# Optimization experiments

Measured on AMD Instinct MI355X. Metric: run time of the kernel, lower is better.

The kernel has to match this reference:

```python
import jax, jax.numpy as jnp
import numpy as np

B, T, C, H, O = 64, 256, 2048, 512, 11
THRESHOLD = 1.0
LEAK = 0.003
OUTPUT_LEAK = LEAK * 0.5


def setup_inputs() -> dict:
    key = jax.random.key(0)
    k1, k2, k3, k4 = jax.random.split(key, 4)
    x = jax.random.normal(k1, (B, T, C), dtype=jnp.float32)
    # xavier_uniform(gain=0.1) for fc1: bound = 0.1*sqrt(6/(C+H))
    b1 = 0.1 * np.sqrt(6.0 / (C + H))
    w1 = jax.random.uniform(k2, (H, C), jnp.float32, -b1, b1)
    # orthogonal(gain=0.1) for fc_rec -> approximate with small gaussian scaled like orthogonal rows
    w_rec = 0.1 * jnp.linalg.qr(jax.random.normal(k3, (H, H), jnp.float32))[0]
    b2 = 0.3 * np.sqrt(6.0 / (H + O))
    w2 = jax.random.uniform(k4, (O, H), jnp.float32, -b2, b2)
    return {"x": x, "w1": w1, "w_rec": w_rec, "w2": w2}


def reference(x, w1, w_rec, w2):
    batch, t_steps, _ = x.shape
    n_hidden = w1.shape[0]
    n_output = w2.shape[0]
    dt = x.dtype

    def step(carry, x_t):
        v1, spk1, v2, out_sum = carry
        # input + recurrent current: [B,H]
        i1 = x_t @ w1.T + spk1 @ w_rec.T
        # subtractive LIF: leak, threshold, subtractive reset
        v1 = v1 + i1 - LEAK
        spk = (v1 >= THRESHOLD).astype(dt)
        v1 = v1 - spk * THRESHOLD
        # non-spiking output accumulator neuron: [B,O]
        i2 = spk @ w2.T
        v2 = jnp.maximum(v2 + i2 - OUTPUT_LEAK, 0.0)
        out_sum = out_sum + v2
        return (v1, spk, v2, out_sum), None

    init = (
        jnp.zeros((batch, n_hidden), dt),
        jnp.zeros((batch, n_hidden), dt),
        jnp.zeros((batch, n_output), dt),
        jnp.zeros((batch, n_output), dt),
    )
    (_, _, _, out_sum), _ = jax.lax.scan(step, init, jnp.swapaxes(x, 0, 1))
    return out_sum / t_steps
```

## Files before the change

kernel.cpp:

```cpp
#include <hip/hip_runtime.h>
#include <cstddef>

#define B_ 64
#define T_ 256
#define C_ 2048
#define H_ 512
#define O_ 11
#define THRESH 1.0f
#define LEAK_ 0.003f
#define OLEAK_ 0.0015f

typedef float v2f __attribute__((ext_vector_type(2)));
typedef float v4f __attribute__((ext_vector_type(4)));

__global__ __launch_bounds__(256) void transpose_wrec(const float* __restrict__ w,
                                                      float* __restrict__ wt) {
    __shared__ float tile[32][33];
    int tx = threadIdx.x, ty = threadIdx.y;
    int x = blockIdx.x * 32 + tx;
    int y = blockIdx.y * 32 + ty;
#pragma unroll
    for (int i = 0; i < 32; i += 8)
        tile[ty + i][tx] = w[(size_t)(y + i) * H_ + x];
    __syncthreads();
    int x2 = blockIdx.y * 32 + tx;
    int y2 = blockIdx.x * 32 + ty;
#pragma unroll
    for (int i = 0; i < 32; i += 8)
        wt[(size_t)(y2 + i) * H_ + x2] = tile[tx][ty + i];
}

#define BM 128
#define BN 128
#define BK 16
#define LDT (BM + 4)

template <int S>
__global__ __launch_bounds__(256) void gemm_ff(const float* __restrict__ A,
                                               const float* __restrict__ Bw,
                                               float* __restrict__ Pout) {
    const int K = C_;
    const int N = H_;
    const int kLen = C_ / S;

    const int i  = blockIdx.x + 4 * blockIdx.y + 512 * blockIdx.z;
    const int l  = (i & 7) * (64 * S) + (i >> 3);
    const int bx = l & 3;
    const int by = (l >> 2) & 127;
    const int bz = l >> 9;

    const int kBase = bz * kLen;

    __shared__ float As[BK][LDT];
    __shared__ float Bs[BK][LDT];

    const int t  = threadIdx.x;
    const int tx = t & 15;
    const int ty = t >> 4;
    const int lr = t >> 2;
    const int lc = (t & 3) * 4;

    const float* Ap = A  + (size_t)(by * BM + lr) * K + kBase + lc;
    const float* Bp = Bw + (size_t)(bx * BN + lr) * K + kBase + lc;

    v2f acc[8][4];
#pragma unroll
    for (int ii = 0; ii < 8; ++ii)
#pragma unroll
        for (int j = 0; j < 4; ++j) acc[ii][j] = (v2f){0.f, 0.f};

    float4 a0 = *(const float4*)(Ap);
    float4 a1 = *(const float4*)(Ap + (size_t)64 * K);
    float4 b0 = *(const float4*)(Bp);
    float4 b1 = *(const float4*)(Bp + (size_t)64 * K);

    for (int k0 = 0;;) {
        __syncthreads();
        As[lc + 0][lr] = a0.x; As[lc + 1][lr] = a0.y;
        As[lc + 2][lr] = a0.z; As[lc + 3][lr] = a0.w;
        As[lc + 0][lr + 64] = a1.x; As[lc + 1][lr + 64] = a1.y;
        As[lc + 2][lr + 64] = a1.z; As[lc + 3][lr + 64] = a1.w;
        Bs[lc + 0][lr] = b0.x; Bs[lc + 1][lr] = b0.y;
        Bs[lc + 2][lr] = b0.z; Bs[lc + 3][lr] = b0.w;
        Bs[lc + 0][lr + 64] = b1.x; Bs[lc + 1][lr + 64] = b1.y;
        Bs[lc + 2][lr + 64] = b1.z; Bs[lc + 3][lr + 64] = b1.w;
        __syncthreads();

        k0 += BK;
        const bool more = (k0 < kLen);
        if (more) {
            Ap += BK; Bp += BK;
            a0 = *(const float4*)(Ap);
            a1 = *(const float4*)(Ap + (size_t)64 * K);
            b0 = *(const float4*)(Bp);
            b1 = *(const float4*)(Bp + (size_t)64 * K);
        }

#pragma unroll
        for (int k = 0; k < BK; ++k) {
            float4 alo = *(const float4*)&As[k][ty * 4];
            float4 ahi = *(const float4*)&As[k][64 + ty * 4];
            float4 blo = *(const float4*)&Bs[k][tx * 4];
            float4 bhi = *(const float4*)&Bs[k][64 + tx * 4];
            v2f b0v = {blo.x, blo.y}, b1v = {blo.z, blo.w};
            v2f b2v = {bhi.x, bhi.y}, b3v = {bhi.z, bhi.w};
            float av[8] = {alo.x, alo.y, alo.z, alo.w, ahi.x, ahi.y, ahi.z, ahi.w};
#pragma unroll
            for (int ii = 0; ii < 8; ++ii) {
                v2f ai = {av[ii], av[ii]};
                acc[ii][0] += ai * b0v;
                acc[ii][1] += ai * b1v;
                acc[ii][2] += ai * b2v;
                acc[ii][3] += ai * b3v;
            }
        }
        if (!more) break;
    }

    float* P = Pout + (size_t)bz * ((size_t)B_ * T_ * H_);
#pragma unroll
    for (int ii = 0; ii < 8; ++ii) {
        int row = by * BM + (ii < 4 ? ty * 4 + ii : 64 + ty * 4 + (ii - 4));
        float* Cp = P + (size_t)row * N + bx * BN;
        v4f c0 = {acc[ii][0].x, acc[ii][0].y, acc[ii][1].x, acc[ii][1].y};
        v4f c1 = {acc[ii][2].x, acc[ii][2].y, acc[ii][3].x, acc[ii][3].y};
        __builtin_nontemporal_store(c0, (v4f*)(Cp + tx * 4));
        __builtin_nontemporal_store(c1, (v4f*)(Cp + 64 + tx * 4));
    }
}

template <int S>
__global__ __launch_bounds__(512) void snn_rec(const float* __restrict__ I1,
                                               const float* __restrict__ wrT,
                                               const float* __restrict__ w2,
                                               float* __restrict__ out) {
    const int b    = blockIdx.x;
    const int h    = threadIdx.x;
    const int lane = h & 63;
    const int w    = h >> 6;

    __shared__ float w2sT[H_ * 12];
    __shared__ int   lists[2][H_];
    __shared__ int   wcnt[8];
    __shared__ float v2s[O_];
    __shared__ float osum[O_];

#pragma unroll
    for (int o = 0; o < O_; ++o) w2sT[h * 12 + o] = w2[o * H_ + h];
    if (h < O_) { v2s[h] = 0.f; osum[h] = 0.f; }

    float v1 = 0.f;
    int   pc = 0;
    const float*  i1p  = I1 + (size_t)b * T_ * H_ + h;
    const float*  wr_h = wrT + h;
    const size_t  PARTF = (size_t)B_ * T_ * H_;

    float pfA[S], pfB[S];
#pragma unroll
    for (int s = 0; s < S; ++s) pfA[s] = __builtin_nontemporal_load(i1p + s * PARTF);
#pragma unroll
    for (int s = 0; s < S; ++s) pfB[s] = __builtin_nontemporal_load(i1p + s * PARTF + H_);
    __syncthreads();

    for (int t = 0; t < T_; ++t) {
        const int cur = t & 1;

        float acc = -LEAK_;
        if (cur == 0) {
#pragma unroll
            for (int s = 0; s < S; ++s) acc += pfA[s];
            const size_t tn = (size_t)((t + 2 < T_) ? t + 2 : t);
#pragma unroll
            for (int s = 0; s < S; ++s)
                pfA[s] = __builtin_nontemporal_load(i1p + s * PARTF + tn * H_);
        } else {
#pragma unroll
            for (int s = 0; s < S; ++s) acc += pfB[s];
            const size_t tn = (size_t)((t + 2 < T_) ? t + 2 : t);
#pragma unroll
            for (int s = 0; s < S; ++s)
                pfB[s] = __builtin_nontemporal_load(i1p + s * PARTF + tn * H_);
        }

        const int* pl = lists[cur ^ 1];
        int j = 0;
        for (; j + 15 < pc; j += 16) {
            const int4 ia = *(const int4*)(pl + j);
            const int4 ib = *(const int4*)(pl + j + 4);
            const int4 ic = *(const int4*)(pl + j + 8);
            const int4 id = *(const int4*)(pl + j + 12);
            float g0 = wr_h[ia.x * H_], g1 = wr_h[ia.y * H_];
            float g2 = wr_h[ia.z * H_], g3 = wr_h[ia.w * H_];
            float g4 = wr_h[ib.x * H_], g5 = wr_h[ib.y * H_];
            float g6 = wr_h[ib.z * H_], g7 = wr_h[ib.w * H_];
            float g8 = wr_h[ic.x * H_], g9 = wr_h[ic.y * H_];
            float gA = wr_h[ic.z * H_], gB = wr_h[ic.w * H_];
            float gC = wr_h[id.x * H_], gD = wr_h[id.y * H_];
            float gE = wr_h[id.z * H_], gF = wr_h[id.w * H_];
            acc += g0; acc += g1; acc += g2; acc += g3;
            acc += g4; acc += g5; acc += g6; acc += g7;
            acc += g8; acc += g9; acc += gA; acc += gB;
            acc += gC; acc += gD; acc += gE; acc += gF;
        }
        for (; j + 7 < pc; j += 8) {
            const int4 ia = *(const int4*)(pl + j);
            const int4 ib = *(const int4*)(pl + j + 4);
            float g0 = wr_h[ia.x * H_], g1 = wr_h[ia.y * H_];
            float g2 = wr_h[ia.z * H_], g3 = wr_h[ia.w * H_];
            float g4 = wr_h[ib.x * H_], g5 = wr_h[ib.y * H_];
            float g6 = wr_h[ib.z * H_], g7 = wr_h[ib.w * H_];
            acc += g0; acc += g1; acc += g2; acc += g3;
            acc += g4; acc += g5; acc += g6; acc += g7;
        }
        for (; j < pc; ++j) acc += wr_h[pl[j] * H_];

        v1 += acc;
        const bool spike = (v1 >= THRESH);
        if (spike) v1 -= THRESH;

        unsigned long long m = __ballot(spike);
        int lb = __popcll(m & ((1ull << lane) - 1ull));
        if (lane == 0) wcnt[w] = (int)__popcll(m);
        __syncthreads();

        int base = 0, tot = 0;
#pragma unroll
        for (int ww = 0; ww < 8; ++ww) {
            int c = wcnt[ww];
            if (ww < w) base += c;
            tot += c;
        }
        if (spike) lists[cur][base + lb] = h;
        __syncthreads();

        if (h < O_) {
            const int* cl = lists[cur];
            float s2 = 0.f;
            for (int j2 = 0; j2 < tot; ++j2) s2 += w2sT[cl[j2] * 12 + h];
            float v2 = v2s[h] + s2 - OLEAK_;
            v2 = v2 > 0.f ? v2 : 0.f;
            v2s[h] = v2;
            osum[h] += v2;
        }
        pc = tot;
    }
    __syncthreads();
    if (h < O_) out[b * O_ + h] = osum[h] * (1.0f / (float)T_);
}

extern "C" void kernel_launch(void* const* d_in, const int* in_sizes, int n_in,
                              void* d_out, int out_size, void* d_ws, size_t ws_size,
                              hipStream_t stream) {
    const float* x     = (const float*)d_in[0];
    const float* w1    = (const float*)d_in[1];
    const float* w_rec = (const float*)d_in[2];
    const float* w2    = (const float*)d_in[3];
    float* out = (float*)d_out;

    const size_t PART = (size_t)B_ * T_ * H_ * sizeof(float);
    const size_t WRT  = (size_t)H_ * H_ * sizeof(float);

    int S = 1;
    if (ws_size >= 4 * PART + WRT) S = 4;
    else if (ws_size >= 2 * PART + WRT) S = 2;

    float* P   = (float*)d_ws;
    float* wrT = (float*)((char*)d_ws + (size_t)S * PART);

    transpose_wrec<<<dim3(H_ / 32, H_ / 32), dim3(32, 8), 0, stream>>>(w_rec, wrT);

    dim3 ggrid(H_ / BN, (B_ * T_) / BM, S);
    switch (S) {
        case 4:
            gemm_ff<4><<<ggrid, dim3(256), 0, stream>>>(x, w1, P);
            snn_rec<4><<<dim3(B_), dim3(H_), 0, stream>>>(P, wrT, w2, out);
            break;
        case 2:
            gemm_ff<2><<<ggrid, dim3(256), 0, stream>>>(x, w1, P);
            snn_rec<2><<<dim3(B_), dim3(H_), 0, stream>>>(P, wrT, w2, out);
            break;
        default:
            gemm_ff<1><<<ggrid, dim3(256), 0, stream>>>(x, w1, P);
            snn_rec<1><<<dim3(B_), dim3(H_), 0, stream>>>(P, wrT, w2, out);
            break;
    }
}
```

Measured before the change: 782.7 us.

## Double-buffer GEMM LDS tiles, simplify recurrent prefetch, use LDS-only barriers

The feed-forward GEMM now ping-pongs between two shared-memory tiles, so each k-step needs one barrier instead of two. It also switches the partial-sum stores from nontemporal to regular stores. The recurrent kernel prefetches the input current one step ahead with normal loads instead of two steps ahead with nontemporal loads. It also replaces __syncthreads with a barrier that waits only on LDS counters, to shorten the per-timestep serial latency. The shallower prefetch may expose global-load latency inside the serial time loop.

```diff
diff --git a/kernel.cpp b/kernel.cpp
--- a/kernel.cpp
+++ b/kernel.cpp
@@ -11,7 +11,11 @@
 #define OLEAK_ 0.0015f
 
 typedef float v2f __attribute__((ext_vector_type(2)));
-typedef float v4f __attribute__((ext_vector_type(4)));
+
+__device__ __forceinline__ void lds_barrier() {
+    asm volatile("s_waitcnt lgkmcnt(0)" ::: "memory");
+    __builtin_amdgcn_s_barrier();
+}
 
 __global__ __launch_bounds__(256) void transpose_wrec(const float* __restrict__ w,
                                                       float* __restrict__ wt) {
@@ -48,11 +52,10 @@
     const int bx = l & 3;
     const int by = (l >> 2) & 127;
     const int bz = l >> 9;
-
     const int kBase = bz * kLen;
 
-    __shared__ float As[BK][LDT];
-    __shared__ float Bs[BK][LDT];
+    __shared__ float As[2][BK][LDT];
+    __shared__ float Bs[2][BK][LDT];
 
     const int t  = threadIdx.x;
     const int tx = t & 15;
@@ -74,34 +77,24 @@
     float4 b0 = *(const float4*)(Bp);
     float4 b1 = *(const float4*)(Bp + (size_t)64 * K);
 
-    for (int k0 = 0;;) {
-        __syncthreads();
-        As[lc + 0][lr] = a0.x; As[lc + 1][lr] = a0.y;
-        As[lc + 2][lr] = a0.z; As[lc + 3][lr] = a0.w;
-        As[lc + 0][lr + 64] = a1.x; As[lc + 1][lr + 64] = a1.y;
-        As[lc + 2][lr + 64] = a1.z; As[lc + 3][lr + 64] = a1.w;
-        Bs[lc + 0][lr] = b0.x; Bs[lc + 1][lr] = b0.y;
-        Bs[lc + 2][lr] = b0.z; Bs[lc + 3][lr] = b0.w;
-        Bs[lc + 0][lr + 64] = b1.x; Bs[lc + 1][lr + 64] = b1.y;
-        Bs[lc + 2][lr + 64] = b1.z; Bs[lc + 3][lr + 64] = b1.w;
-        __syncthreads();
-
-        k0 += BK;
-        const bool more = (k0 < kLen);
-        if (more) {
-            Ap += BK; Bp += BK;
-            a0 = *(const float4*)(Ap);
-            a1 = *(const float4*)(Ap + (size_t)64 * K);
-            b0 = *(const float4*)(Bp);
-            b1 = *(const float4*)(Bp + (size_t)64 * K);
-        }
-
+    auto stage = [&](int pb) {
+        As[pb][lc + 0][lr] = a0.x; As[pb][lc + 1][lr] = a0.y;
+        As[pb][lc + 2][lr] = a0.z; As[pb][lc + 3][lr] = a0.w;
+        As[pb][lc + 0][lr + 64] = a1.x; As[pb][lc + 1][lr + 64] = a1.y;
+        As[pb][lc + 2][lr + 64] = a1.z; As[pb][lc + 3][lr + 64] = a1.w;
+        Bs[pb][lc + 0][lr] = b0.x; Bs[pb][lc + 1][lr] = b0.y;
+        Bs[pb][lc + 2][lr] = b0.z; Bs[pb][lc + 3][lr] = b0.w;
+        Bs[pb][lc + 0][lr + 64] = b1.x; Bs[pb][lc + 1][lr + 64] = b1.y;
+        Bs[pb][lc + 2][lr + 64] = b1.z; Bs[pb][lc + 3][lr + 64] = b1.w;
+    };
+
+    auto compute = [&](int pb) {
 #pragma unroll
         for (int k = 0; k < BK; ++k) {
-            float4 alo = *(const float4*)&As[k][ty * 4];
-            float4 ahi = *(const float4*)&As[k][64 + ty * 4];
-            float4 blo = *(const float4*)&Bs[k][tx * 4];
-            float4 bhi = *(const float4*)&Bs[k][64 + tx * 4];
+            float4 alo = *(const float4*)&As[pb][k][ty * 4];
+            float4 ahi = *(const float4*)&As[pb][k][64 + ty * 4];
+            float4 blo = *(const float4*)&Bs[pb][k][tx * 4];
+            float4 bhi = *(const float4*)&Bs[pb][k][64 + tx * 4];
             v2f b0v = {blo.x, blo.y}, b1v = {blo.z, blo.w};
             v2f b2v = {bhi.x, bhi.y}, b3v = {bhi.z, bhi.w};
             float av[8] = {alo.x, alo.y, alo.z, alo.w, ahi.x, ahi.y, ahi.z, ahi.w};
@@ -114,18 +107,34 @@
                 acc[ii][3] += ai * b3v;
             }
         }
-        if (!more) break;
-    }
+    };
+
+    stage(0);
+    __syncthreads();
+
+    int p = 0;
+    for (int k0 = BK; k0 < kLen; k0 += BK) {
+        Ap += BK; Bp += BK;
+        a0 = *(const float4*)(Ap);
+        a1 = *(const float4*)(Ap + (size_t)64 * K);
+        b0 = *(const float4*)(Bp);
+        b1 = *(const float4*)(Bp + (size_t)64 * K);
+        compute(p);
+        stage(p ^ 1);
+        lds_barrier();
+        p ^= 1;
+    }
+    compute(p);
 
     float* P = Pout + (size_t)bz * ((size_t)B_ * T_ * H_);
 #pragma unroll
     for (int ii = 0; ii < 8; ++ii) {
         int row = by * BM + (ii < 4 ? ty * 4 + ii : 64 + ty * 4 + (ii - 4));
         float* Cp = P + (size_t)row * N + bx * BN;
-        v4f c0 = {acc[ii][0].x, acc[ii][0].y, acc[ii][1].x, acc[ii][1].y};
-        v4f c1 = {acc[ii][2].x, acc[ii][2].y, acc[ii][3].x, acc[ii][3].y};
-        __builtin_nontemporal_store(c0, (v4f*)(Cp + tx * 4));
-        __builtin_nontemporal_store(c1, (v4f*)(Cp + 64 + tx * 4));
+        float4 c0 = {acc[ii][0].x, acc[ii][0].y, acc[ii][1].x, acc[ii][1].y};
+        float4 c1 = {acc[ii][2].x, acc[ii][2].y, acc[ii][3].x, acc[ii][3].y};
+        *(float4*)(Cp + tx * 4)      = c0;
+        *(float4*)(Cp + 64 + tx * 4) = c1;
     }
 }
 
@@ -155,32 +164,21 @@
     const float*  wr_h = wrT + h;
     const size_t  PARTF = (size_t)B_ * T_ * H_;
 
-    float pfA[S], pfB[S];
-#pragma unroll
-    for (int s = 0; s < S; ++s) pfA[s] = __builtin_nontemporal_load(i1p + s * PARTF);
-#pragma unroll
-    for (int s = 0; s < S; ++s) pfB[s] = __builtin_nontemporal_load(i1p + s * PARTF + H_);
+    float pf[S];
+#pragma unroll
+    for (int s = 0; s < S; ++s) pf[s] = i1p[s * PARTF];
     __syncthreads();
 
     for (int t = 0; t < T_; ++t) {
         const int cur = t & 1;
 
         float acc = -LEAK_;
-        if (cur == 0) {
-#pragma unroll
-            for (int s = 0; s < S; ++s) acc += pfA[s];
-            const size_t tn = (size_t)((t + 2 < T_) ? t + 2 : t);
-#pragma unroll
-            for (int s = 0; s < S; ++s)
-                pfA[s] = __builtin_nontemporal_load(i1p + s * PARTF + tn * H_);
-        } else {
-#pragma unroll
-            for (int s = 0; s < S; ++s) acc += pfB[s];
-            const size_t tn = (size_t)((t + 2 < T_) ? t + 2 : t);
-#pragma unroll
-            for (int s = 0; s < S; ++s)
-                pfB[s] = __builtin_nontemporal_load(i1p + s * PARTF + tn * H_);
-        }
+#pragma unroll
+        for (int s = 0; s < S; ++s) acc += pf[s];
+
+        const int tn = (t + 1 < T_) ? t + 1 : t;
+#pragma unroll
+        for (int s = 0; s < S; ++s) pf[s] = i1p[s * PARTF + (size_t)tn * H_];
 
         const int* pl = lists[cur ^ 1];
         int j = 0;
@@ -221,7 +219,7 @@
         unsigned long long m = __ballot(spike);
         int lb = __popcll(m & ((1ull << lane) - 1ull));
         if (lane == 0) wcnt[w] = (int)__popcll(m);
-        __syncthreads();
+        lds_barrier();
 
         int base = 0, tot = 0;
 #pragma unroll
@@ -231,7 +229,7 @@
             tot += c;
         }
         if (spike) lists[cur][base + lb] = h;
-        __syncthreads();
+        lds_barrier();
 
         if (h < O_) {
             const int* cl = lists[cur];
```

Result: faster. 744.2 us (-4.9%).
